# Performance work log

Measured on AMD Instinct MI355X. Metric: run time of the kernel, lower is better.

The kernel has to match this reference:

```python
import jax, jax.numpy as jnp
import numpy as np

DIM = 768
NUM_HEAD = 12
DIM_HEAD = DIM // NUM_HEAD
SCALE = DIM_HEAD ** -0.5
B, N = 4, 1024


def setup_inputs() -> dict:
    key = jax.random.key(0)
    ks = jax.random.split(key, 6)
    return {
        "x": jax.random.normal(ks[0], (B, N, DIM), jnp.float32),
        "q_weight": jax.random.normal(ks[1], (DIM, DIM), jnp.float32) * 0.02,
        "k_weight": jax.random.normal(ks[2], (DIM, DIM), jnp.float32) * 0.02,
        "v_weight": jax.random.normal(ks[3], (DIM, DIM), jnp.float32) * 0.02,
        "q_bias": jnp.zeros((DIM,), jnp.float32),
        "k_bias": jnp.zeros((DIM,), jnp.float32),
        "v_bias": jnp.zeros((DIM,), jnp.float32),
        "proj_weight": jax.random.normal(ks[4], (DIM, DIM), jnp.float32) * 0.02,
        "proj_bias": jax.random.normal(ks[5], (DIM,), jnp.float32) * 0.02,
    }


def reference(x, q_weight, k_weight, v_weight, q_bias, k_bias, v_bias,
              proj_weight, proj_bias):
    B_, N_, C = x.shape
    shortcut = x
    # pre-norm: torch .std() is unbiased (ddof=1)
    mean = jnp.mean(x, axis=-1, keepdims=True)
    std = jnp.std(x, axis=-1, keepdims=True, ddof=1)
    xn = (x - mean) / std
    # F.linear: x @ W.T + b
    q = xn @ q_weight.T + q_bias
    k = xn @ k_weight.T + k_bias
    v = xn @ v_weight.T + v_bias
    # b n (h d) -> b h n d
    q = q.reshape(B_, N_, NUM_HEAD, DIM_HEAD).transpose(0, 2, 1, 3)
    k = k.reshape(B_, N_, NUM_HEAD, DIM_HEAD).transpose(0, 2, 1, 3)
    v = v.reshape(B_, N_, NUM_HEAD, DIM_HEAD).transpose(0, 2, 1, 3)
    attn = jnp.einsum('bhqd,bhkd->bhqk', q, k * SCALE)
    attn = jax.nn.softmax(attn, axis=-1)
    out = jnp.einsum('bhqk,bhkd->bhqd', attn, v)
    out = out.transpose(0, 2, 1, 3).reshape(B_, N_, C)
    out = out @ proj_weight.T + proj_bias
    return out + shortcut
```

## Files before the change

### kernel.cpp

```cpp
#include <hip/hip_runtime.h>

typedef unsigned short ushort_t;
typedef unsigned int uint_t;
typedef __attribute__((ext_vector_type(8))) unsigned short ushort8;
typedef __attribute__((ext_vector_type(2))) unsigned int uint2v;
typedef __attribute__((ext_vector_type(8))) __bf16 bf16x8;
typedef __attribute__((ext_vector_type(4))) float floatx4;

#define DIM 768
#define NHEAD 12
#define DHEAD 64
#define SEQ 1024
#define BATCH 4
#define TOKENS (BATCH * SEQ)
#define WELEM (DIM * DIM)
#define SCALE_LOG2E 0.18033688011112042f

static __device__ __forceinline__ uint_t fbits(float f) {
  union { float f; uint_t u; } c; c.f = f; return c.u;
}
static __device__ __forceinline__ ushort_t f2bf(float f) {
  return (ushort_t)((fbits(f) + 0x8000u) >> 16);
}
static __device__ __forceinline__ uint_t pack_bf2(float lo, float hi) {
  const uint_t a = fbits(lo) + 0x8000u, b = fbits(hi) + 0x8000u;
#if __has_builtin(__builtin_amdgcn_perm)
  return __builtin_amdgcn_perm(b, a, 0x07060302u);
#else
  return (a >> 16) | (b & 0xFFFF0000u);
#endif
}
static __device__ __forceinline__ float fexp2(float x) {
#if __has_builtin(__builtin_amdgcn_exp2f)
  return __builtin_amdgcn_exp2f(x);
#else
  return exp2f(x);
#endif
}
static __device__ __forceinline__ floatx4 mfma16(ushort8 a, ushort8 b, floatx4 c) {
  return __builtin_amdgcn_mfma_f32_16x16x32_bf16(
      __builtin_bit_cast(bf16x8, a), __builtin_bit_cast(bf16x8, b), c, 0, 0, 0);
}
static __device__ __forceinline__ void gload_lds16(const ushort_t* g,
                                                   ushort_t* l) {
  __builtin_amdgcn_global_load_lds(
      (const __attribute__((address_space(1))) void*)g,
      (__attribute__((address_space(3))) void*)l, 16, 0, 0);
}

__global__ __launch_bounds__(256) void prep_kernel(
    const float* __restrict__ qw, const float* __restrict__ kw,
    const float* __restrict__ vw, const float* __restrict__ pw,
    const float* __restrict__ x, ushort_t* __restrict__ wbf,
    ushort_t* __restrict__ xn) {
  const int bid = blockIdx.x;
  if (bid < 2304) {
    const int mat = bid / 576, inner = bid % 576;
    const float* s = (mat == 0) ? qw : (mat == 1) ? kw : (mat == 2) ? vw : pw;
    ushort_t* d = wbf + (size_t)mat * WELEM;
    const int i = (inner * 256 + threadIdx.x) * 4;
    const float4 f = *(const float4*)&s[i];
    uint2v o;
    o[0] = pack_bf2(f.x, f.y);
    o[1] = pack_bf2(f.z, f.w);
    *(uint2v*)&d[i] = o;
  } else {
    const int wave = threadIdx.x >> 6, lane = threadIdx.x & 63;
    const int row = (bid - 2304) * 4 + wave;
    const float4* xr = (const float4*)(x + (size_t)row * DIM);
    float4 v[3];
    float s = 0.f, s2 = 0.f;
#pragma unroll
    for (int j = 0; j < 3; ++j) {
      v[j] = xr[j * 64 + lane];
      s += v[j].x + v[j].y + v[j].z + v[j].w;
      s2 += v[j].x * v[j].x + v[j].y * v[j].y + v[j].z * v[j].z +
            v[j].w * v[j].w;
    }
#pragma unroll
    for (int off = 1; off < 64; off <<= 1) {
      s += __shfl_xor(s, off);
      s2 += __shfl_xor(s2, off);
    }
    const float mean = s * (1.f / 768.f);
    const float var = (s2 - 768.f * mean * mean) * (1.f / 767.f);
    const float rstd = rsqrtf(var);
    ushort_t* xo = xn + (size_t)row * DIM;
#pragma unroll
    for (int j = 0; j < 3; ++j) {
      uint2v o;
      o[0] = pack_bf2((v[j].x - mean) * rstd, (v[j].y - mean) * rstd);
      o[1] = pack_bf2((v[j].z - mean) * rstd, (v[j].w - mean) * rstd);
      *(uint2v*)&xo[(j * 64 + lane) * 4] = o;
    }
  }
}

#define BK 64
#define NKIT (DIM / BK)
__global__ __launch_bounds__(256) void qkv_kernel(
    const ushort_t* __restrict__ xn, const ushort_t* __restrict__ wbf,
    const float* __restrict__ qb, const float* __restrict__ kb,
    const float* __restrict__ vb,
    ushort_t* __restrict__ qh, ushort_t* __restrict__ kh,
    ushort_t* __restrict__ vt) {
  __shared__ ushort_t As[2][64 * BK];
  __shared__ ushort_t Bs[2][128 * BK];
  const int tid = threadIdx.x;
  const int wave = tid >> 6, lane = tid & 63, quad = lane >> 4, l15 = lane & 15;
  const int m0 = blockIdx.x * 64;
  const int mat = blockIdx.y / 6, nb = blockIdx.y % 6;
  const int n0 = nb * 128;
  const ushort_t* W = wbf + (size_t)mat * WELEM;
  const int chan_off = (wave >> 1) * 64, tok_off = (wave & 1) * 32;
  const int srow8 = lane >> 3;
  const int schunk = (lane & 7) ^ srow8;
  const int l7 = l15 & 7;

  floatx4 acc[4][2];
#pragma unroll
  for (int i = 0; i < 4; ++i)
#pragma unroll
    for (int j = 0; j < 2; ++j) acc[i][j] = (floatx4){0.f, 0.f, 0.f, 0.f};

  auto stage = [&](int k0, int bf) {
#pragma unroll
    for (int i = 0; i < 2; ++i) {
      const int c = wave * 2 + i;
      gload_lds16(&xn[(size_t)(m0 + c * 8 + srow8) * DIM + k0 + schunk * 8],
                  &As[bf][c * 512]);
    }
#pragma unroll
    for (int i = 0; i < 4; ++i) {
      const int c = wave * 4 + i;
      gload_lds16(&W[(size_t)(n0 + c * 8 + srow8) * DIM + k0 + schunk * 8],
                  &Bs[bf][c * 512]);
    }
  };

  stage(0, 0);
  for (int it = 0; it < NKIT; ++it) {
    const int cur = it & 1;
    __syncthreads();
    if (it + 1 < NKIT) stage((it + 1) * BK, cur ^ 1);
    ushort8 af[2][2], bfr[4][2];
#pragma unroll
    for (int k2 = 0; k2 < 2; ++k2) {
      const int ch = ((k2 * 4 + quad) ^ l7) * 8;
#pragma unroll
      for (int j = 0; j < 2; ++j)
        af[j][k2] = *(const ushort8*)&As[cur][(tok_off + j * 16 + l15) * BK + ch];
#pragma unroll
      for (int i = 0; i < 4; ++i)
        bfr[i][k2] = *(const ushort8*)&Bs[cur][(chan_off + i * 16 + l15) * BK + ch];
    }
#pragma unroll
    for (int k2 = 0; k2 < 2; ++k2)
#pragma unroll
      for (int i = 0; i < 4; ++i)
#pragma unroll
        for (int j = 0; j < 2; ++j)
          acc[i][j] = mfma16(bfr[i][k2], af[j][k2], acc[i][j]);
  }

  if (mat != 2) {
    const float* bias = (mat == 0) ? qb : kb;
    ushort_t* dst = (mat == 0) ? qh : kh;
    const float os = (mat == 0) ? SCALE_LOG2E : 1.0f;
    const int hh = (n0 + chan_off) >> 6;
#pragma unroll
    for (int i = 0; i < 4; ++i) {
      const int ch0 = n0 + chan_off + i * 16 + quad * 4;
      const float4 bv = *(const float4*)&bias[ch0];
      const int d0 = i * 16 + quad * 4;
#pragma unroll
      for (int j = 0; j < 2; ++j) {
        const int tok = m0 + tok_off + j * 16 + l15;
        const int bb = tok >> 10, nn = tok & 1023;
        uint2v pk;
        pk[0] = pack_bf2((acc[i][j][0] + bv.x) * os, (acc[i][j][1] + bv.y) * os);
        pk[1] = pack_bf2((acc[i][j][2] + bv.z) * os, (acc[i][j][3] + bv.w) * os);
        *(uint2v*)&dst[(size_t)((bb * NHEAD + hh) * SEQ + nn) * DHEAD + d0] = pk;
      }
    }
  } else {
    const int tokg = m0 + tok_off;
    const int bb = tokg >> 10, gg = tokg & 1023;
#pragma unroll
    for (int i = 0; i < 4; ++i) {
      const int ch0 = n0 + chan_off + i * 16 + quad * 4;
      const float4 bv = *(const float4*)&vb[ch0];
      const float bvf[4] = {bv.x, bv.y, bv.z, bv.w};
      const int hh = ch0 >> 6, d0 = ch0 & 63;
#pragma unroll
      for (int r = 0; r < 4; ++r) {
        const size_t base = (size_t)((bb * NHEAD + hh) * DHEAD + d0 + r) * SEQ;
        *(uint_t*)&vt[base + gg + l15 * 2] =
            pack_bf2(acc[i][0][r] + bvf[r], acc[i][1][r] + bvf[r]);
      }
    }
  }
}

#define PSTR2 34
__global__ __launch_bounds__(256) void attn_kernel(
    const ushort_t* __restrict__ qh, const ushort_t* __restrict__ kh,
    const ushort_t* __restrict__ vt, ushort_t* __restrict__ ao) {
  __shared__ ushort_t kv[2][2][2][2048];
  __shared__ ushort_t Ps[4][2][16 * PSTR2];
  float* cb = (float*)&kv[0][0][0][0];
  const int tid = threadIdx.x;
  const int wave = tid >> 6, lane = tid & 63, quad = lane >> 4, l15 = lane & 15;
  const int l7 = l15 & 7;
  const int grp = wave >> 1, wsub = wave & 1;
  const int bid = blockIdx.x;
  const int idx = bid >> 3;
  const int hb = (bid & 7) * 6 + idx % 6;
  const int qb = idx / 6;
  const int h = hb % NHEAD, b = hb / NHEAD;
  const int basekv = ((b * NHEAD + h) * SEQ) * DHEAD;
  const int basevt = ((b * NHEAD + h) * DHEAD) * SEQ;
  const int q0 = qb * 64 + wsub * 32;
  const int kbase = grp * 512;

  ushort8 qf[2][2];
#pragma unroll
  for (int w = 0; w < 2; ++w) {
    const ushort_t* Qr = qh + basekv + (q0 + w * 16 + l15) * DHEAD;
    qf[w][0] = *(const ushort8*)&Qr[quad * 8];
    qf[w][1] = *(const ushort8*)&Qr[32 + quad * 8];
  }
  ushort8 ones;
#pragma unroll
  for (int i = 0; i < 8; ++i) ones[i] = 0x3F80;

  floatx4 o[2][4];
#pragma unroll
  for (int w = 0; w < 2; ++w)
#pragma unroll
    for (int t = 0; t < 4; ++t) o[w][t] = (floatx4){0.f, 0.f, 0.f, 0.f};
  floatx4 acc_l[2] = {(floatx4){0.f, 0.f, 0.f, 0.f},
                      (floatx4){0.f, 0.f, 0.f, 0.f}};

  const int ksrow = lane >> 3, kschunk = (lane & 7) ^ ksrow;
  const int vdrow = lane >> 2;
  const int vchunk = (lane & 3) ^ ((vdrow >> 1) & 3);

  auto stage = [&](int kt, int bf) {
#pragma unroll
    for (int i = 0; i < 2; ++i) {
      const int c = wsub * 2 + i;
      gload_lds16(&kh[basekv + (kt + c * 8 + ksrow) * DHEAD + kschunk * 8],
                  &kv[grp][bf][0][c * 512]);
      gload_lds16(&vt[basevt + (c * 16 + vdrow) * SEQ + kt + vchunk * 8],
                  &kv[grp][bf][1][c * 512]);
    }
  };

  stage(kbase, 0);
  for (int it = 0; it < 16; ++it) {
    const int cur = it & 1;
    __syncthreads();
    if (it + 1 < 16) stage(kbase + (it + 1) * 32, cur ^ 1);
    const ushort_t* K = &kv[grp][cur][0][0];
    const ushort_t* V = &kv[grp][cur][1][0];

    floatx4 sacc[2][2];
#pragma unroll
    for (int w = 0; w < 2; ++w)
#pragma unroll
      for (int s = 0; s < 2; ++s) sacc[w][s] = (floatx4){0.f, 0.f, 0.f, 0.f};
#pragma unroll
    for (int s = 0; s < 2; ++s) {
#pragma unroll
      for (int hh = 0; hh < 2; ++hh) {
        const ushort8 kf = *(const ushort8*)&K[(s * 16 + l15) * 64 +
                                               (((hh * 4 + quad) ^ l7) * 8)];
#pragma unroll
        for (int w = 0; w < 2; ++w)
          sacc[w][s] = mfma16(qf[w][hh], kf, sacc[w][s]);
      }
    }

#pragma unroll
    for (int w = 0; w < 2; ++w)
#pragma unroll
      for (int r = 0; r < 4; ++r)
        *(uint_t*)&Ps[wave][w][(quad * 4 + r) * PSTR2 + l15 * 2] =
            pack_bf2(fexp2(sacc[w][0][r]), fexp2(sacc[w][1][r]));

    ushort8 pf[2];
#pragma unroll
    for (int w = 0; w < 2; ++w) {
      pf[w] = *(const ushort8*)&Ps[wave][w][l15 * PSTR2 + quad * 8];
      acc_l[w] = mfma16(pf[w], ones, acc_l[w]);
    }
#pragma unroll
    for (int t = 0; t < 4; ++t) {
      const ushort8 vf = *(const ushort8*)&V[(t * 16 + l15) * 32 +
                                             ((quad ^ ((l15 >> 1) & 3)) * 8)];
#pragma unroll
      for (int w = 0; w < 2; ++w) o[w][t] = mfma16(pf[w], vf, o[w][t]);
    }
  }
  __syncthreads();

  const int cb0 = wsub * (32 * 66);
  if (grp == 1) {
#pragma unroll
    for (int w = 0; w < 2; ++w) {
#pragma unroll
      for (int t = 0; t < 4; ++t)
#pragma unroll
        for (int r = 0; r < 4; ++r)
          cb[cb0 + (w * 16 + quad * 4 + r) * 66 + t * 16 + l15] = o[w][t][r];
      if (l15 == 0)
#pragma unroll
        for (int r = 0; r < 4; ++r)
          cb[cb0 + (w * 16 + quad * 4 + r) * 66 + 64] = acc_l[w][r];
    }
  }
  __syncthreads();
  if (grp == 0) {
#pragma unroll
    for (int w = 0; w < 2; ++w) {
#pragma unroll
      for (int r = 0; r < 4; ++r) {
        const int row = w * 16 + quad * 4 + r;
        const float l = acc_l[w][r] + cb[cb0 + row * 66 + 64];
        const float rl = 1.f / l;
        const int token = b * SEQ + q0 + row;
#pragma unroll
        for (int t = 0; t < 4; ++t) {
          const float val = o[w][t][r] + cb[cb0 + row * 66 + t * 16 + l15];
          ao[(size_t)token * DIM + h * DHEAD + t * 16 + l15] = f2bf(val * rl);
        }
      }
    }
  }
}

__global__ __launch_bounds__(256) void proj_kernel(
    const ushort_t* __restrict__ ao, const ushort_t* __restrict__ pwb,
    const float* __restrict__ pb, const float* __restrict__ x,
    float* __restrict__ out) {
  __shared__ ushort_t As[2][64 * BK];
  __shared__ ushort_t Bs[2][128 * BK];
  const int tid = threadIdx.x;
  const int wave = tid >> 6, lane = tid & 63, quad = lane >> 4, l15 = lane & 15;
  const int m0 = blockIdx.x * 64;
  const int n0 = blockIdx.y * 128;
  const int chan_off = (wave >> 1) * 64, tok_off = (wave & 1) * 32;
  const int srow8 = lane >> 3;
  const int schunk = (lane & 7) ^ srow8;
  const int l7 = l15 & 7;

  floatx4 acc[4][2];
#pragma unroll
  for (int i = 0; i < 4; ++i)
#pragma unroll
    for (int j = 0; j < 2; ++j) acc[i][j] = (floatx4){0.f, 0.f, 0.f, 0.f};

  auto stage = [&](int k0, int bf) {
#pragma unroll
    for (int i = 0; i < 2; ++i) {
      const int c = wave * 2 + i;
      gload_lds16(&ao[(size_t)(m0 + c * 8 + srow8) * DIM + k0 + schunk * 8],
                  &As[bf][c * 512]);
    }
#pragma unroll
    for (int i = 0; i < 4; ++i) {
      const int c = wave * 4 + i;
      gload_lds16(&pwb[(size_t)(n0 + c * 8 + srow8) * DIM + k0 + schunk * 8],
                  &Bs[bf][c * 512]);
    }
  };

  stage(0, 0);
  for (int it = 0; it < NKIT; ++it) {
    const int cur = it & 1;
    __syncthreads();
    if (it + 1 < NKIT) stage((it + 1) * BK, cur ^ 1);
    ushort8 af[2][2], bfr[4][2];
#pragma unroll
    for (int k2 = 0; k2 < 2; ++k2) {
      const int ch = ((k2 * 4 + quad) ^ l7) * 8;
#pragma unroll
      for (int j = 0; j < 2; ++j)
        af[j][k2] = *(const ushort8*)&As[cur][(tok_off + j * 16 + l15) * BK + ch];
#pragma unroll
      for (int i = 0; i < 4; ++i)
        bfr[i][k2] = *(const ushort8*)&Bs[cur][(chan_off + i * 16 + l15) * BK + ch];
    }
#pragma unroll
    for (int k2 = 0; k2 < 2; ++k2)
#pragma unroll
      for (int i = 0; i < 4; ++i)
#pragma unroll
        for (int j = 0; j < 2; ++j)
          acc[i][j] = mfma16(bfr[i][k2], af[j][k2], acc[i][j]);
  }

#pragma unroll
  for (int i = 0; i < 4; ++i) {
    const int ch0 = n0 + chan_off + i * 16 + quad * 4;
    const float4 bv = *(const float4*)&pb[ch0];
#pragma unroll
    for (int j = 0; j < 2; ++j) {
      const int tok = m0 + tok_off + j * 16 + l15;
      const float4 res = *(const float4*)&x[(size_t)tok * DIM + ch0];
      float4 ov;
      ov.x = acc[i][j][0] + bv.x + res.x;
      ov.y = acc[i][j][1] + bv.y + res.y;
      ov.z = acc[i][j][2] + bv.z + res.z;
      ov.w = acc[i][j][3] + bv.w + res.w;
      *(float4*)&out[(size_t)tok * DIM + ch0] = ov;
    }
  }
}

extern "C" void kernel_launch(void* const* d_in, const int* in_sizes, int n_in,
                              void* d_out, int out_size, void* d_ws,
                              size_t ws_size, hipStream_t stream) {
  const float* x  = (const float*)d_in[0];
  const float* qw = (const float*)d_in[1];
  const float* kw = (const float*)d_in[2];
  const float* vw = (const float*)d_in[3];
  const float* qb = (const float*)d_in[4];
  const float* kb = (const float*)d_in[5];
  const float* vb = (const float*)d_in[6];
  const float* pw = (const float*)d_in[7];
  const float* pb = (const float*)d_in[8];
  float* out = (float*)d_out;

  ushort_t* ws = (ushort_t*)d_ws;
  const size_t NTOK = (size_t)TOKENS * DIM;
  ushort_t* xn  = ws;
  ushort_t* qh  = ws + NTOK;
  ushort_t* kh  = ws + 2 * NTOK;
  ushort_t* vt  = ws + 3 * NTOK;
  ushort_t* wbf = ws + 4 * NTOK;
  ushort_t* ao  = xn;

  prep_kernel<<<2304 + TOKENS / 4, 256, 0, stream>>>(qw, kw, vw, pw, x, wbf, xn);
  qkv_kernel<<<dim3(64, 18), 256, 0, stream>>>(xn, wbf, qb, kb, vb, qh, kh, vt);
  attn_kernel<<<768, 256, 0, stream>>>(qh, kh, vt, ao);
  proj_kernel<<<dim3(64, 6), 256, 0, stream>>>(ao, wbf + 3 * (size_t)WELEM, pb,
                                               x, out);
}
```

Measured before the change: 153.6 us.

## Add producer-wave ring pipeline to QKV GEMM and shrink proj tile

The QKV GEMM gains a fifth wave that acts as a dedicated loader, filling a 3-stage LDS ring and signalling the four compute waves through shared-memory flag and done counters instead of block-wide barriers. This aims to overlap global-to-LDS loads with MFMA work and remove __syncthreads stalls. Separately, the projection GEMM tile drops from 64x128 to 64x64, doubling its grid to 768 blocks for better CU occupancy. Risks include spin-wait overhead, fragile hand-coded waitcnt encodings, a single loader wave becoming the bottleneck, and the bounded spin loops silently timing out.

```diff
diff --git a/kernel.cpp b/kernel.cpp
--- a/kernel.cpp
+++ b/kernel.cpp
@@ -98,61 +98,84 @@
 
 #define BK 64
 #define NKIT (DIM / BK)
-__global__ __launch_bounds__(256) void qkv_kernel(
+#define RING 3
+__global__ __launch_bounds__(320) void qkv_kernel(
     const ushort_t* __restrict__ xn, const ushort_t* __restrict__ wbf,
     const float* __restrict__ qb, const float* __restrict__ kb,
     const float* __restrict__ vb,
     ushort_t* __restrict__ qh, ushort_t* __restrict__ kh,
     ushort_t* __restrict__ vt) {
-  __shared__ ushort_t As[2][64 * BK];
-  __shared__ ushort_t Bs[2][128 * BK];
+  __shared__ ushort_t As[RING][64 * BK];
+  __shared__ ushort_t Bs[RING][128 * BK];
+  __shared__ int flag[RING];
+  __shared__ int done[RING];
   const int tid = threadIdx.x;
   const int wave = tid >> 6, lane = tid & 63, quad = lane >> 4, l15 = lane & 15;
   const int m0 = blockIdx.x * 64;
   const int mat = blockIdx.y / 6, nb = blockIdx.y % 6;
   const int n0 = nb * 128;
   const ushort_t* W = wbf + (size_t)mat * WELEM;
-  const int chan_off = (wave >> 1) * 64, tok_off = (wave & 1) * 32;
   const int srow8 = lane >> 3;
   const int schunk = (lane & 7) ^ srow8;
   const int l7 = l15 & 7;
 
+  if (tid < RING) { flag[tid] = 0; done[tid] = 0; }
+  __syncthreads();
+
+  if (wave == 4) {
+    for (int t = 0; t <= NKIT; ++t) {
+      if (t < NKIT) {
+        if (t >= RING) {
+          const int need = 4 * (t / RING);
+          int g = 0;
+          while (__atomic_load_n(&done[t % RING], __ATOMIC_RELAXED) < need &&
+                 ++g < (1 << 22)) {}
+        }
+        const int k0 = t * BK, s = t % RING;
+#pragma unroll
+        for (int c = 0; c < 8; ++c)
+          gload_lds16(&xn[(size_t)(m0 + c * 8 + srow8) * DIM + k0 + schunk * 8],
+                      &As[s][c * 512]);
+#pragma unroll
+        for (int c = 0; c < 16; ++c)
+          gload_lds16(&W[(size_t)(n0 + c * 8 + srow8) * DIM + k0 + schunk * 8],
+                      &Bs[s][c * 512]);
+      }
+      if (t >= 1) {
+        if (t < NKIT)
+          __builtin_amdgcn_s_waitcnt(0x4F78);
+        else
+          __builtin_amdgcn_s_waitcnt(0x0F70);
+        __atomic_store_n(&flag[(t - 1) % RING], t, __ATOMIC_RELAXED);
+      }
+    }
+    return;
+  }
+
+  const int chan_off = (wave >> 1) * 64, tok_off = (wave & 1) * 32;
   floatx4 acc[4][2];
 #pragma unroll
   for (int i = 0; i < 4; ++i)
 #pragma unroll
     for (int j = 0; j < 2; ++j) acc[i][j] = (floatx4){0.f, 0.f, 0.f, 0.f};
 
-  auto stage = [&](int k0, int bf) {
-#pragma unroll
-    for (int i = 0; i < 2; ++i) {
-      const int c = wave * 2 + i;
-      gload_lds16(&xn[(size_t)(m0 + c * 8 + srow8) * DIM + k0 + schunk * 8],
-                  &As[bf][c * 512]);
-    }
-#pragma unroll
-    for (int i = 0; i < 4; ++i) {
-      const int c = wave * 4 + i;
-      gload_lds16(&W[(size_t)(n0 + c * 8 + srow8) * DIM + k0 + schunk * 8],
-                  &Bs[bf][c * 512]);
-    }
-  };
-
-  stage(0, 0);
-  for (int it = 0; it < NKIT; ++it) {
-    const int cur = it & 1;
-    __syncthreads();
-    if (it + 1 < NKIT) stage((it + 1) * BK, cur ^ 1);
+  for (int t = 0; t < NKIT; ++t) {
+    const int s = t % RING;
+    {
+      int g = 0;
+      while (__atomic_load_n(&flag[s], __ATOMIC_RELAXED) < t + 1 &&
+             ++g < (1 << 22)) {}
+    }
     ushort8 af[2][2], bfr[4][2];
 #pragma unroll
     for (int k2 = 0; k2 < 2; ++k2) {
       const int ch = ((k2 * 4 + quad) ^ l7) * 8;
 #pragma unroll
       for (int j = 0; j < 2; ++j)
-        af[j][k2] = *(const ushort8*)&As[cur][(tok_off + j * 16 + l15) * BK + ch];
+        af[j][k2] = *(const ushort8*)&As[s][(tok_off + j * 16 + l15) * BK + ch];
 #pragma unroll
       for (int i = 0; i < 4; ++i)
-        bfr[i][k2] = *(const ushort8*)&Bs[cur][(chan_off + i * 16 + l15) * BK + ch];
+        bfr[i][k2] = *(const ushort8*)&Bs[s][(chan_off + i * 16 + l15) * BK + ch];
     }
 #pragma unroll
     for (int k2 = 0; k2 < 2; ++k2)
@@ -161,6 +184,8 @@
 #pragma unroll
         for (int j = 0; j < 2; ++j)
           acc[i][j] = mfma16(bfr[i][k2], af[j][k2], acc[i][j]);
+    __builtin_amdgcn_s_waitcnt(0xC07F);
+    __atomic_fetch_add(&done[s], 1, __ATOMIC_RELAXED);
   }
 
   if (mat != 2) {
@@ -344,20 +369,20 @@
     const ushort_t* __restrict__ ao, const ushort_t* __restrict__ pwb,
     const float* __restrict__ pb, const float* __restrict__ x,
     float* __restrict__ out) {
-  __shared__ ushort_t As[2][64 * BK];
-  __shared__ ushort_t Bs[2][128 * BK];
+  __shared__ ushort_t Asp[2][64 * BK];
+  __shared__ ushort_t Bsp[2][64 * BK];
   const int tid = threadIdx.x;
   const int wave = tid >> 6, lane = tid & 63, quad = lane >> 4, l15 = lane & 15;
   const int m0 = blockIdx.x * 64;
-  const int n0 = blockIdx.y * 128;
-  const int chan_off = (wave >> 1) * 64, tok_off = (wave & 1) * 32;
+  const int n0 = blockIdx.y * 64;
+  const int chan_off = (wave >> 1) * 32, tok_off = (wave & 1) * 32;
   const int srow8 = lane >> 3;
   const int schunk = (lane & 7) ^ srow8;
   const int l7 = l15 & 7;
 
-  floatx4 acc[4][2];
-#pragma unroll
-  for (int i = 0; i < 4; ++i)
+  floatx4 acc[2][2];
+#pragma unroll
+  for (int i = 0; i < 2; ++i)
 #pragma unroll
     for (int j = 0; j < 2; ++j) acc[i][j] = (floatx4){0.f, 0.f, 0.f, 0.f};
 
@@ -366,13 +391,13 @@
     for (int i = 0; i < 2; ++i) {
       const int c = wave * 2 + i;
       gload_lds16(&ao[(size_t)(m0 + c * 8 + srow8) * DIM + k0 + schunk * 8],
-                  &As[bf][c * 512]);
-    }
-#pragma unroll
-    for (int i = 0; i < 4; ++i) {
-      const int c = wave * 4 + i;
+                  &Asp[bf][c * 512]);
+    }
+#pragma unroll
+    for (int i = 0; i < 2; ++i) {
+      const int c = wave * 2 + i;
       gload_lds16(&pwb[(size_t)(n0 + c * 8 + srow8) * DIM + k0 + schunk * 8],
-                  &Bs[bf][c * 512]);
+                  &Bsp[bf][c * 512]);
     }
   };
 
@@ -381,28 +406,28 @@
     const int cur = it & 1;
     __syncthreads();
     if (it + 1 < NKIT) stage((it + 1) * BK, cur ^ 1);
-    ushort8 af[2][2], bfr[4][2];
+    ushort8 af[2][2], bfr[2][2];
 #pragma unroll
     for (int k2 = 0; k2 < 2; ++k2) {
       const int ch = ((k2 * 4 + quad) ^ l7) * 8;
 #pragma unroll
       for (int j = 0; j < 2; ++j)
-        af[j][k2] = *(const ushort8*)&As[cur][(tok_off + j * 16 + l15) * BK + ch];
-#pragma unroll
-      for (int i = 0; i < 4; ++i)
-        bfr[i][k2] = *(const ushort8*)&Bs[cur][(chan_off + i * 16 + l15) * BK + ch];
+        af[j][k2] = *(const ushort8*)&Asp[cur][(tok_off + j * 16 + l15) * BK + ch];
+#pragma unroll
+      for (int i = 0; i < 2; ++i)
+        bfr[i][k2] = *(const ushort8*)&Bsp[cur][(chan_off + i * 16 + l15) * BK + ch];
     }
 #pragma unroll
     for (int k2 = 0; k2 < 2; ++k2)
 #pragma unroll
-      for (int i = 0; i < 4; ++i)
+      for (int i = 0; i < 2; ++i)
 #pragma unroll
         for (int j = 0; j < 2; ++j)
           acc[i][j] = mfma16(bfr[i][k2], af[j][k2], acc[i][j]);
   }
 
 #pragma unroll
-  for (int i = 0; i < 4; ++i) {
+  for (int i = 0; i < 2; ++i) {
     const int ch0 = n0 + chan_off + i * 16 + quad * 4;
     const float4 bv = *(const float4*)&pb[ch0];
 #pragma unroll
@@ -443,8 +468,8 @@
   ushort_t* ao  = xn;
 
   prep_kernel<<<2304 + TOKENS / 4, 256, 0, stream>>>(qw, kw, vw, pw, x, wbf, xn);
-  qkv_kernel<<<dim3(64, 18), 256, 0, stream>>>(xn, wbf, qb, kb, vb, qh, kh, vt);
+  qkv_kernel<<<dim3(64, 18), 320, 0, stream>>>(xn, wbf, qb, kb, vb, qh, kh, vt);
   attn_kernel<<<768, 256, 0, stream>>>(qh, kh, vt, ao);
-  proj_kernel<<<dim3(64, 6), 256, 0, stream>>>(ao, wbf + 3 * (size_t)WELEM, pb,
-                                               x, out);
-}
+  proj_kernel<<<dim3(64, 12), 256, 0, stream>>>(ao, wbf + 3 * (size_t)WELEM, pb,
+                                                x, out);
+}
```

Result: slower. 172.7 us (+12.4%).
